# Kernel optimization log

Measured on AMD Instinct MI355X. Metric: run time of the kernel, lower is better.

Reference implementation:

```python
import jax, jax.numpy as jnp
import numpy as np

N_NODES = 50000
N_EDGES = 800000
IN_DIM = 128
HID = 128
MLP_DIMS = [512, 256]


def setup_inputs() -> dict:
    key = jax.random.key(0)
    ks = jax.random.split(key, 12)
    x = jax.random.normal(ks[0], (N_NODES, IN_DIM), dtype=jnp.float32)
    edge_index = jax.random.randint(ks[1], (2, N_EDGES), 0, N_NODES, dtype=jnp.int64)
    s = 1.0 / np.sqrt(HID)
    inp = {"x": x, "edge_index": edge_index}
    # 3 GCN layers: 128->128, 128->128, 128->128
    dims_in = [IN_DIM, HID, HID]
    for i, di in enumerate(dims_in):
        inp[f"Wg{i}"] = jax.random.normal(ks[2 + i], (di, HID), dtype=jnp.float32) * (1.0 / np.sqrt(di))
        inp[f"bg{i}"] = jnp.zeros((HID,), dtype=jnp.float32)
    # MLP head: 128->512->256, ReLU after each Linear
    mlp_in = [HID, MLP_DIMS[0]]
    for i, (di, do) in enumerate(zip(mlp_in, MLP_DIMS)):
        inp[f"Wm{i}"] = jax.random.normal(ks[6 + i], (di, do), dtype=jnp.float32) * (1.0 / np.sqrt(di))
        inp[f"bm{i}"] = jnp.zeros((do,), dtype=jnp.float32)
    return inp


def _gcn_prep(edge_index, n):
    # add self-loops (PyG GCNConv default), compute symmetric normalization
    loops = jnp.arange(n, dtype=edge_index.dtype)
    src = jnp.concatenate([edge_index[0], loops])
    dst = jnp.concatenate([edge_index[1], loops])
    deg = jax.ops.segment_sum(jnp.ones_like(src, dtype=jnp.float32), dst, num_segments=n)
    dinv = jax.lax.rsqrt(deg)  # deg >= 1 due to self-loops
    norm = dinv[src] * dinv[dst]  # [E+N]
    return src, dst, norm


def _gcn_layer(x, W, b, src, dst, norm, n):
    h = x @ W  # [N, HID]
    msg = h[src] * norm[:, None]  # gather + scale, [E+N, HID]
    out = jax.ops.segment_sum(msg, dst, num_segments=n)  # scatter-add
    return out + b


def reference(x, edge_index, Wg0, bg0, Wg1, bg1, Wg2, bg2, Wm0, bm0, Wm1, bm1):
    n = x.shape[0]
    src, dst, norm = _gcn_prep(edge_index, n)
    h = x
    for W, b in ((Wg0, bg0), (Wg1, bg1), (Wg2, bg2)):
        h = jax.nn.relu(_gcn_layer(h, W, b, src, dst, norm, n))
    # MLP head (ends with ReLU: pop() only removed the trailing Dropout)
    h = jax.nn.relu(h @ Wm0 + bm0)
    h = jax.nn.relu(h @ Wm1 + bm1)
    return h
```

## Files before the change

### kernel.cpp

```cpp
#include <hip/hip_runtime.h>

#define HID 128
#define NCHUNK 4

typedef _Float16 half8 __attribute__((ext_vector_type(8)));
typedef _Float16 half4h __attribute__((ext_vector_type(4)));
using float4v = __attribute__((ext_vector_type(4))) float;

typedef const __attribute__((address_space(1))) unsigned int* gas_ptr;
typedef __attribute__((address_space(3))) unsigned int* las_ptr;
__device__ __forceinline__ void gld16(const void* g, void* l) {
    __builtin_amdgcn_global_load_lds((gas_ptr)g, (las_ptr)l, 16, 0, 0);
}

__device__ __forceinline__ int chunk_of(int s, int CH) {
    return (s >= CH) + (s >= 2 * CH) + (s >= 3 * CH);
}

struct WSegs {
    const float* W[5];
    _Float16* H[5];
    int K[5], M[5], start[5];
};

__global__ __launch_bounds__(256) void fused_prep1(
    const int* __restrict__ src, const int* __restrict__ dst,
    int* __restrict__ degc, int E, int nDeg, int CH,
    const float* __restrict__ x, _Float16* __restrict__ Xh, int total4, int nX,
    WSegs S, int totalW) {
    int bx = blockIdx.x;
    if (bx < nDeg) {
        int i = bx * 256 + (int)threadIdx.x;
        if (i < E) {
            int d = dst[i];
            int p = chunk_of(src[i], CH);
            atomicAdd(&degc[4 * d + p], 1);
        }
    } else if (bx < nDeg + nX) {
        int i = (bx - nDeg) * 256 + (int)threadIdx.x;
        if (i >= total4) return;
        const float4 v = *(const float4*)(x + (size_t)i * 4);
        half4h h;
        h.x = (_Float16)v.x; h.y = (_Float16)v.y; h.z = (_Float16)v.z; h.w = (_Float16)v.w;
        *(half4h*)(Xh + (size_t)i * 4) = h;
    } else {
        int idx = (bx - nDeg - nX) * 256 + (int)threadIdx.x;
        if (idx >= totalW) return;
        int s = 0;
#pragma unroll
        for (int t = 1; t < 5; ++t)
            if (idx >= S.start[t]) s = t;
        int local = idx - S.start[s];
        int M = S.M[s], K = S.K[s];
        int k = local / M;
        int m = local - k * M;
        S.H[s][(size_t)m * K + k] = (_Float16)S.W[s][local];
    }
}

__global__ __launch_bounds__(256) void prep2_kernel(
    const int* __restrict__ degc, int* __restrict__ rowbeg,
    int* __restrict__ cursor, float* __restrict__ dinv, int* __restrict__ tot, int N4) {
    int e = blockIdx.x * 256 + (int)threadIdx.x;
    int lane = (int)threadIdx.x & 63;
    int d = (e < N4) ? degc[e] : 0;
    int incl = d;
#pragma unroll
    for (int off = 1; off < 64; off <<= 1) {
        int t = __shfl_up(incl, off, 64);
        if (lane >= off) incl += t;
    }
    int wsum = __shfl(incl, 63, 64);
    int wbase = 0;
    if (lane == 63) wbase = atomicAdd(tot, wsum);
    wbase = __shfl(wbase, 63, 64);
    int d4 = d;
    d4 += __shfl_xor(d4, 1, 64);
    d4 += __shfl_xor(d4, 2, 64);
    if (e < N4) {
        int b = wbase + incl - d;
        rowbeg[e] = b;
        cursor[e] = b;
        if ((lane & 3) == 0) dinv[e >> 2] = rsqrtf((float)d4 + 1.0f);
    }
}

template <bool SCALE, bool BIAS, bool RELU, bool OUTHALF>
__device__ __forceinline__ void gemm_body(
    int bxc, int byr, const _Float16* __restrict__ Ah, const _Float16* __restrict__ Bh,
    const float* __restrict__ bias, const float* __restrict__ rowscale,
    float* __restrict__ outF, _Float16* __restrict__ outH, int Nout, int K, int M,
    _Float16* lds) {
    const int tid = threadIdx.x;
    const int bm = byr * 64;
    const int bn = bxc * 128;
    const int wave = tid >> 6, lane = tid & 63;
    const int quad = lane >> 4, c16 = lane & 15;
    const int wn = wave * 32;

    float4v acc[4][2];
#pragma unroll
    for (int a = 0; a < 4; ++a)
#pragma unroll
        for (int b = 0; b < 2; ++b)
#pragma unroll
            for (int r = 0; r < 4; ++r) acc[a][b][r] = 0.0f;

    const int r0 = tid >> 2;
    const int kq0 = (tid & 3) * 8;

    const _Float16* gA  = Ah + (size_t)(bm + r0) * K + kq0;
    const _Float16* gB0 = Bh + (size_t)(bn + r0) * K + kq0;
    const _Float16* gB1 = Bh + (size_t)(bn + r0 + 64) * K + kq0;

    auto issue = [&](int c) {
        _Float16* buf = lds + (size_t)(c & 1) * 6144;
        int k0 = c * 32;
        gld16(gA + k0, buf + (size_t)tid * 8);
        gld16(gB0 + k0, buf + 2048 + (size_t)tid * 8);
        gld16(gB1 + k0, buf + 2048 + (size_t)(tid + 256) * 8);
    };

    issue(0);
    __syncthreads();

    const int nch = K >> 5;
    for (int c = 0; c < nch; ++c) {
        if (c + 1 < nch) issue(c + 1);

        const _Float16* buf = lds + (size_t)(c & 1) * 6144;
        half8 af[4], bf[2];
#pragma unroll
        for (int t = 0; t < 4; ++t)
            af[t] = *(const half8*)&buf[(t * 16 + c16) * 32 + quad * 8];
#pragma unroll
        for (int t = 0; t < 2; ++t)
            bf[t] = *(const half8*)&buf[2048 + (wn + t * 16 + c16) * 32 + quad * 8];
#pragma unroll
        for (int tm = 0; tm < 4; ++tm)
#pragma unroll
            for (int tn = 0; tn < 2; ++tn)
                acc[tm][tn] = __builtin_amdgcn_mfma_f32_16x16x32_f16(af[tm], bf[tn], acc[tm][tn], 0, 0, 0);
        __syncthreads();
    }

#pragma unroll
    for (int tm = 0; tm < 4; ++tm) {
#pragma unroll
        for (int tn = 0; tn < 2; ++tn) {
            int colg = bn + wn + tn * 16 + c16;
            float bv = BIAS ? bias[colg] : 0.0f;
#pragma unroll
            for (int r = 0; r < 4; ++r) {
                int row = bm + tm * 16 + quad * 4 + r;
                if (row >= Nout) continue;
                float v = acc[tm][tn][r];
                if (SCALE) v *= rowscale[row];
                if (BIAS) v += bv;
                if (RELU) v = fmaxf(v, 0.0f);
                if (OUTHALF) outH[(size_t)row * M + colg] = (_Float16)v;
                else         outF[(size_t)row * M + colg] = v;
            }
        }
    }
}

template <bool SCALE, bool BIAS, bool RELU, bool OUTHALF>
__global__ __launch_bounds__(256, 4) void gemm_std(
    const _Float16* __restrict__ Ah, const _Float16* __restrict__ Bh,
    const float* __restrict__ bias, const float* __restrict__ rowscale,
    float* __restrict__ outF, _Float16* __restrict__ outH, int Nout, int K, int M) {
    __shared__ _Float16 lds[2 * 6144];
    gemm_body<SCALE, BIAS, RELU, OUTHALF>(blockIdx.x, blockIdx.y, Ah, Bh, bias, rowscale,
                                          outF, outH, Nout, K, M, lds);
}

__global__ __launch_bounds__(256, 4) void fill_gemm_kernel(
    const int* __restrict__ src, const int* __restrict__ dst,
    int* __restrict__ cursor, int* __restrict__ col, int E, int nFill, int CH,
    const _Float16* __restrict__ Ah, const _Float16* __restrict__ Bh,
    const float* __restrict__ rowscale, _Float16* __restrict__ outH,
    int Nout, int K, int M) {
    __shared__ _Float16 lds[2 * 6144];
    int bx = blockIdx.x;
    if (bx < nFill) {
        int e = bx * 256 + (int)threadIdx.x;
        if (e < E) {
            int d = dst[e];
            int s = src[e];
            int p = chunk_of(s, CH);
            int pos = atomicAdd(&cursor[4 * d + p], 1);
            col[pos] = s;
        }
    } else {
        gemm_body<true, false, false, true>(0, bx - nFill, Ah, Bh, nullptr, rowscale,
                                            nullptr, outH, Nout, K, M, lds);
    }
}

__global__ __launch_bounds__(256) void gather_kernel(
    const _Float16* __restrict__ hs, const int* __restrict__ rowbeg,
    const int* __restrict__ rowend, const int* __restrict__ col,
    const float* __restrict__ dinv, const float* __restrict__ bias,
    _Float16* __restrict__ Ch, int N) {
    long long idx = (long long)blockIdx.x * blockDim.x + threadIdx.x;
    int i = (int)(idx >> 4);
    if (i >= N) return;
    int c = ((int)idx & 15) * 8;

    const int4 rbv = *(const int4*)(rowbeg + (size_t)4 * i);
    const int4 rev = *(const int4*)(rowend + (size_t)4 * i);
    int jb[4] = {rbv.x, rbv.y, rbv.z, rbv.w};
    int je[4] = {rev.x, rev.y, rev.z, rev.w};

    const half8 sv = *(const half8*)(hs + (size_t)i * HID + c);
    float ax[8];
#pragma unroll
    for (int r = 0; r < 8; ++r) ax[r] = (float)sv[r];

#pragma unroll
    for (int p = 0; p < 4; ++p) {
        int j = jb[p];
        const int end = je[p];
        for (; j + 8 <= end; j += 8) {
            int s0 = col[j],     s1 = col[j + 1], s2 = col[j + 2], s3 = col[j + 3];
            int s4 = col[j + 4], s5 = col[j + 5], s6 = col[j + 6], s7 = col[j + 7];
            const half8 v0 = *(const half8*)(hs + (size_t)s0 * HID + c);
            const half8 v1 = *(const half8*)(hs + (size_t)s1 * HID + c);
            const half8 v2 = *(const half8*)(hs + (size_t)s2 * HID + c);
            const half8 v3 = *(const half8*)(hs + (size_t)s3 * HID + c);
            const half8 v4 = *(const half8*)(hs + (size_t)s4 * HID + c);
            const half8 v5 = *(const half8*)(hs + (size_t)s5 * HID + c);
            const half8 v6 = *(const half8*)(hs + (size_t)s6 * HID + c);
            const half8 v7 = *(const half8*)(hs + (size_t)s7 * HID + c);
#pragma unroll
            for (int r = 0; r < 8; ++r)
                ax[r] += (((float)v0[r] + (float)v1[r]) + ((float)v2[r] + (float)v3[r])) +
                         (((float)v4[r] + (float)v5[r]) + ((float)v6[r] + (float)v7[r]));
        }
        for (; j + 4 <= end; j += 4) {
            int s0 = col[j], s1 = col[j + 1], s2 = col[j + 2], s3 = col[j + 3];
            const half8 v0 = *(const half8*)(hs + (size_t)s0 * HID + c);
            const half8 v1 = *(const half8*)(hs + (size_t)s1 * HID + c);
            const half8 v2 = *(const half8*)(hs + (size_t)s2 * HID + c);
            const half8 v3 = *(const half8*)(hs + (size_t)s3 * HID + c);
#pragma unroll
            for (int r = 0; r < 8; ++r)
                ax[r] += ((float)v0[r] + (float)v1[r]) + ((float)v2[r] + (float)v3[r]);
        }
        for (; j < end; ++j) {
            int s = col[j];
            const half8 v = *(const half8*)(hs + (size_t)s * HID + c);
#pragma unroll
            for (int r = 0; r < 8; ++r) ax[r] += (float)v[r];
        }
    }

    float di = dinv[i];
    half8 rr;
#pragma unroll
    for (int r = 0; r < 8; ++r)
        rr[r] = (_Float16)fmaxf(ax[r] * di + bias[c + r], 0.0f);
    *(half8*)(Ch + (size_t)i * HID + c) = rr;
}


extern "C" void kernel_launch(void* const* d_in, const int* in_sizes, int n_in,
                              void* d_out, int out_size, void* d_ws, size_t ws_size,
                              hipStream_t stream) {
    const float* x   = (const float*)d_in[0];
    const int*   ei  = (const int*)d_in[1];
    const float* Wg0 = (const float*)d_in[2];
    const float* bg0 = (const float*)d_in[3];
    const float* Wg1 = (const float*)d_in[4];
    const float* bg1 = (const float*)d_in[5];
    const float* Wg2 = (const float*)d_in[6];
    const float* bg2 = (const float*)d_in[7];
    const float* Wm0 = (const float*)d_in[8];
    const float* bm0 = (const float*)d_in[9];
    const float* Wm1 = (const float*)d_in[10];
    const float* bm1 = (const float*)d_in[11];
    float* out = (float*)d_out;

    const int N  = in_sizes[0] / HID;
    const int E  = in_sizes[1] / 2;
    const int M0 = in_sizes[9];
    const int M1 = in_sizes[11];
    const int Npad = ((N + 127) / 128) * 128;
    const int CH = (N + NCHUNK - 1) / NCHUNK;
    const int N4 = 4 * N;

    const int* src = ei;
    const int* dst = ei + E;

    char* ws = (char*)d_ws;
    size_t off = 0;
    auto alloc = [&](size_t bytes) {
        void* p = ws + off;
        off += (bytes + 255) & ~(size_t)255;
        return p;
    };
    int* degc   = (int*)alloc((size_t)N4 * 4);
    int* tot    = (int*)alloc(256);
    int* rowbeg = (int*)alloc((size_t)N4 * 4);
    int* cursor = (int*)alloc((size_t)N4 * 4);
    int* colbuf = (int*)alloc((size_t)E * 4);
    float* dinv = (float*)alloc((size_t)N * 4);
    _Float16* WgT[3];
    for (int l = 0; l < 3; ++l)
        WgT[l] = (_Float16*)alloc((size_t)HID * HID * 2);
    _Float16* Wm0T = (_Float16*)alloc((size_t)M0 * HID * 2);
    _Float16* Wm1T = (_Float16*)alloc((size_t)M1 * M0 * 2);
    _Float16* Xh = (_Float16*)alloc((size_t)Npad * HID * 2);
    _Float16* Hs = (_Float16*)alloc((size_t)Npad * HID * 2);
    _Float16* Ch = (_Float16*)alloc((size_t)Npad * HID * 2);
    _Float16* Mh = (_Float16*)alloc((size_t)Npad * M0 * 2);

    hipMemsetAsync(degc, 0, ((char*)tot - (char*)degc) + 256, stream);

    const int nDeg = (E + 255) / 256;
    const int total4 = N * HID / 4;
    const int nX = (total4 + 255) / 256;
    int totalW;
    WSegs S;
    {
        const float* Ws[5] = {Wg0, Wg1, Wg2, Wm0, Wm1};
        _Float16* Hs5[5]   = {WgT[0], WgT[1], WgT[2], Wm0T, Wm1T};
        int Ks[5] = {HID, HID, HID, HID, M0};
        int Ms[5] = {HID, HID, HID, M0, M1};
        int start = 0;
        for (int s = 0; s < 5; ++s) {
            S.W[s] = Ws[s]; S.H[s] = Hs5[s];
            S.K[s] = Ks[s]; S.M[s] = Ms[s]; S.start[s] = start;
            start += Ks[s] * Ms[s];
        }
        totalW = start;
    }
    const int nW = (totalW + 255) / 256;
    fused_prep1<<<nDeg + nX + nW, 256, 0, stream>>>(
        src, dst, degc, E, nDeg, CH, x, Xh, total4, nX, S, totalW);

    prep2_kernel<<<(N4 + 255) / 256, 256, 0, stream>>>(
        degc, rowbeg, cursor, dinv, tot, N4);

    fill_gemm_kernel<<<nDeg + Npad / 64, 256, 0, stream>>>(
        src, dst, cursor, colbuf, E, nDeg, CH,
        Xh, WgT[0], dinv, Hs, N, HID, HID);

    const float* bg[3] = {bg0, bg1, bg2};
    long long gatherThreads = (long long)N * 16;
    int gblocks = (int)((gatherThreads + 255) / 256);
    gather_kernel<<<gblocks, 256, 0, stream>>>(
        Hs, rowbeg, cursor, colbuf, dinv, bg[0], Ch, N);
    for (int l = 1; l < 3; ++l) {
        gemm_std<true, false, false, true><<<dim3(1, Npad / 64), 256, 0, stream>>>(
            Ch, WgT[l], nullptr, dinv, nullptr, Hs, N, HID, HID);
        gather_kernel<<<gblocks, 256, 0, stream>>>(
            Hs, rowbeg, cursor, colbuf, dinv, bg[l], Ch, N);
    }

    gemm_std<false, true, true, true><<<dim3(M0 / 128, Npad / 64), 256, 0, stream>>>(
        Ch, Wm0T, bm0, nullptr, nullptr, Mh, N, HID, M0);
    gemm_std<false, true, true, false><<<dim3(M1 / 128, Npad / 64), 256, 0, stream>>>(
        Mh, Wm1T, bm1, nullptr, out, nullptr, N, M0, M1);
}
```

Baseline: 446.4 us.

## Partition CSR fill by destination range per XCD, stage GEMM output via LDS

The fill phase now assigns each group of blocks (by blockIdx modulo 8, matching the XCD round-robin) a destination-node range. Each group scans all edges and only does the atomics for its own range, so cursor atomics and col writes stay local to one XCD's L2. The cost is eight reads of the edge lists, done with nontemporal loads. The half-precision GEMM epilogue now writes to LDS and then stores coalesced 16-byte rows instead of scattered 2-byte stores. The gather kernel also uses nontemporal loads for the index arrays and a nontemporal store for its output.

```diff
diff --git a/kernel.cpp b/kernel.cpp
--- a/kernel.cpp
+++ b/kernel.cpp
@@ -2,9 +2,11 @@
 
 #define HID 128
 #define NCHUNK 4
+#define NXCD 8
 
 typedef _Float16 half8 __attribute__((ext_vector_type(8)));
 typedef _Float16 half4h __attribute__((ext_vector_type(4)));
+typedef int int4v __attribute__((ext_vector_type(4)));
 using float4v = __attribute__((ext_vector_type(4))) float;
 
 typedef const __attribute__((address_space(1))) unsigned int* gas_ptr;
@@ -144,22 +146,53 @@
         __syncthreads();
     }
 
-#pragma unroll
-    for (int tm = 0; tm < 4; ++tm) {
-#pragma unroll
-        for (int tn = 0; tn < 2; ++tn) {
-            int colg = bn + wn + tn * 16 + c16;
-            float bv = BIAS ? bias[colg] : 0.0f;
-#pragma unroll
-            for (int r = 0; r < 4; ++r) {
-                int row = bm + tm * 16 + quad * 4 + r;
-                if (row >= Nout) continue;
-                float v = acc[tm][tn][r];
-                if (SCALE) v *= rowscale[row];
-                if (BIAS) v += bv;
-                if (RELU) v = fmaxf(v, 0.0f);
-                if (OUTHALF) outH[(size_t)row * M + colg] = (_Float16)v;
-                else         outF[(size_t)row * M + colg] = v;
+    if (OUTHALF) {
+        const int LDT = 136;
+#pragma unroll
+        for (int tm = 0; tm < 4; ++tm) {
+#pragma unroll
+            for (int tn = 0; tn < 2; ++tn) {
+                int coll = wn + tn * 16 + c16;
+                float bv = BIAS ? bias[bn + coll] : 0.0f;
+#pragma unroll
+                for (int r = 0; r < 4; ++r) {
+                    int rowl = tm * 16 + quad * 4 + r;
+                    float v = acc[tm][tn][r];
+                    if (SCALE) v *= rowscale[bm + rowl];
+                    if (BIAS) v += bv;
+                    if (RELU) v = fmaxf(v, 0.0f);
+                    lds[rowl * LDT + coll] = (_Float16)v;
+                }
+            }
+        }
+        __syncthreads();
+#pragma unroll
+        for (int k = 0; k < 4; ++k) {
+            int w = tid * 4 + k;
+            int rowl = w >> 4;
+            int c8 = (w & 15) * 8;
+            int grow = bm + rowl;
+            if (grow < Nout)
+                *(half8*)(outH + (size_t)grow * M + bn + c8) =
+                    *(const half8*)&lds[rowl * LDT + c8];
+        }
+    } else {
+#pragma unroll
+        for (int tm = 0; tm < 4; ++tm) {
+#pragma unroll
+            for (int tn = 0; tn < 2; ++tn) {
+                int colg = bn + wn + tn * 16 + c16;
+                float bv = BIAS ? bias[colg] : 0.0f;
+#pragma unroll
+                for (int r = 0; r < 4; ++r) {
+                    int row = bm + tm * 16 + quad * 4 + r;
+                    if (row >= Nout) continue;
+                    float v = acc[tm][tn][r];
+                    if (SCALE) v *= rowscale[row];
+                    if (BIAS) v += bv;
+                    if (RELU) v = fmaxf(v, 0.0f);
+                    outF[(size_t)row * M + colg] = v;
+                }
             }
         }
     }
@@ -177,20 +210,26 @@
 
 __global__ __launch_bounds__(256, 4) void fill_gemm_kernel(
     const int* __restrict__ src, const int* __restrict__ dst,
-    int* __restrict__ cursor, int* __restrict__ col, int E, int nFill, int CH,
+    int* __restrict__ cursor, int* __restrict__ col, int E, int nFill, int CH, int RANGE,
     const _Float16* __restrict__ Ah, const _Float16* __restrict__ Bh,
     const float* __restrict__ rowscale, _Float16* __restrict__ outH,
     int Nout, int K, int M) {
     __shared__ _Float16 lds[2 * 6144];
     int bx = blockIdx.x;
     if (bx < nFill) {
-        int e = bx * 256 + (int)threadIdx.x;
-        if (e < E) {
-            int d = dst[e];
-            int s = src[e];
-            int p = chunk_of(s, CH);
-            int pos = atomicAdd(&cursor[4 * d + p], 1);
-            col[pos] = s;
+        const int g = bx & (NXCD - 1);
+        const int rb = bx >> 3;
+        const int BPG = nFill >> 3;
+        const int lo = g * RANGE, hi = lo + RANGE;
+        const int stride = BPG * 256;
+        for (int e = rb * 256 + (int)threadIdx.x; e < E; e += stride) {
+            int d = __builtin_nontemporal_load(dst + e);
+            if (d >= lo && d < hi) {
+                int s = __builtin_nontemporal_load(src + e);
+                int p = chunk_of(s, CH);
+                int pos = atomicAdd(&cursor[4 * d + p], 1);
+                col[pos] = s;
+            }
         }
     } else {
         gemm_body<true, false, false, true>(0, bx - nFill, Ah, Bh, nullptr, rowscale,
@@ -208,8 +247,8 @@
     if (i >= N) return;
     int c = ((int)idx & 15) * 8;
 
-    const int4 rbv = *(const int4*)(rowbeg + (size_t)4 * i);
-    const int4 rev = *(const int4*)(rowend + (size_t)4 * i);
+    const int4v rbv = __builtin_nontemporal_load((const int4v*)(rowbeg + (size_t)4 * i));
+    const int4v rev = __builtin_nontemporal_load((const int4v*)(rowend + (size_t)4 * i));
     int jb[4] = {rbv.x, rbv.y, rbv.z, rbv.w};
     int je[4] = {rev.x, rev.y, rev.z, rev.w};
 
@@ -223,8 +262,14 @@
         int j = jb[p];
         const int end = je[p];
         for (; j + 8 <= end; j += 8) {
-            int s0 = col[j],     s1 = col[j + 1], s2 = col[j + 2], s3 = col[j + 3];
-            int s4 = col[j + 4], s5 = col[j + 5], s6 = col[j + 6], s7 = col[j + 7];
+            int s0 = __builtin_nontemporal_load(col + j);
+            int s1 = __builtin_nontemporal_load(col + j + 1);
+            int s2 = __builtin_nontemporal_load(col + j + 2);
+            int s3 = __builtin_nontemporal_load(col + j + 3);
+            int s4 = __builtin_nontemporal_load(col + j + 4);
+            int s5 = __builtin_nontemporal_load(col + j + 5);
+            int s6 = __builtin_nontemporal_load(col + j + 6);
+            int s7 = __builtin_nontemporal_load(col + j + 7);
             const half8 v0 = *(const half8*)(hs + (size_t)s0 * HID + c);
             const half8 v1 = *(const half8*)(hs + (size_t)s1 * HID + c);
             const half8 v2 = *(const half8*)(hs + (size_t)s2 * HID + c);
@@ -239,7 +284,10 @@
                          (((float)v4[r] + (float)v5[r]) + ((float)v6[r] + (float)v7[r]));
         }
         for (; j + 4 <= end; j += 4) {
-            int s0 = col[j], s1 = col[j + 1], s2 = col[j + 2], s3 = col[j + 3];
+            int s0 = __builtin_nontemporal_load(col + j);
+            int s1 = __builtin_nontemporal_load(col + j + 1);
+            int s2 = __builtin_nontemporal_load(col + j + 2);
+            int s3 = __builtin_nontemporal_load(col + j + 3);
             const half8 v0 = *(const half8*)(hs + (size_t)s0 * HID + c);
             const half8 v1 = *(const half8*)(hs + (size_t)s1 * HID + c);
             const half8 v2 = *(const half8*)(hs + (size_t)s2 * HID + c);
@@ -249,7 +297,7 @@
                 ax[r] += ((float)v0[r] + (float)v1[r]) + ((float)v2[r] + (float)v3[r]);
         }
         for (; j < end; ++j) {
-            int s = col[j];
+            int s = __builtin_nontemporal_load(col + j);
             const half8 v = *(const half8*)(hs + (size_t)s * HID + c);
 #pragma unroll
             for (int r = 0; r < 8; ++r) ax[r] += (float)v[r];
@@ -261,7 +309,7 @@
 #pragma unroll
     for (int r = 0; r < 8; ++r)
         rr[r] = (_Float16)fmaxf(ax[r] * di + bias[c + r], 0.0f);
-    *(half8*)(Ch + (size_t)i * HID + c) = rr;
+    __builtin_nontemporal_store(rr, (half8*)(Ch + (size_t)i * HID + c));
 }
 
 
@@ -288,6 +336,7 @@
     const int M1 = in_sizes[11];
     const int Npad = ((N + 127) / 128) * 128;
     const int CH = (N + NCHUNK - 1) / NCHUNK;
+    const int RANGE = (N + NXCD - 1) / NXCD;
     const int N4 = 4 * N;
 
     const int* src = ei;
@@ -316,7 +365,7 @@
     _Float16* Ch = (_Float16*)alloc((size_t)Npad * HID * 2);
     _Float16* Mh = (_Float16*)alloc((size_t)Npad * M0 * 2);
 
-    hipMemsetAsync(degc, 0, ((char*)tot - (char*)degc) + 256, stream);
+    (void)hipMemsetAsync(degc, 0, ((char*)tot - (char*)degc) + 256, stream);
 
     const int nDeg = (E + 255) / 256;
     const int total4 = N * HID / 4;
@@ -343,8 +392,9 @@
     prep2_kernel<<<(N4 + 255) / 256, 256, 0, stream>>>(
         degc, rowbeg, cursor, dinv, tot, N4);
 
-    fill_gemm_kernel<<<nDeg + Npad / 64, 256, 0, stream>>>(
-        src, dst, cursor, colbuf, E, nDeg, CH,
+    const int nFill = ((nDeg + NXCD - 1) / NXCD) * NXCD;
+    fill_gemm_kernel<<<nFill + Npad / 64, 256, 0, stream>>>(
+        src, dst, cursor, colbuf, E, nFill, CH, RANGE,
         Xh, WgT[0], dinv, Hs, N, HID, HID);
 
     const float* bg[3] = {bg0, bg1, bg2};
```

Result: slower. 475.6 us (+6.5%).
